# Optimization experiments

Measured on AMD Instinct MI355X. Metric: run time of the kernel, lower is better.

Reference implementation:

```python
import jax, jax.numpy as jnp
import numpy as np

H = 64
NA, NB, NM, NC = 65536, 131072, 16384, 2048
EDGES = {  # name: (E, n_src, n_dst)
    'aa': (786432, NA, NA), 'ab': (262144, NA, NB), 'am': (262144, NA, NM),
    'bb': (786432, NB, NB), 'bm': (524288, NB, NM), 'mm': (131072, NM, NM),
    'ac': (65536,  NA, NC), 'bc': (131072, NB, NC), 'mc': (16384,  NM, NC),
}
REL_ORDER = ['aa', 'ab', 'am', 'bb', 'bm', 'mm', 'ac', 'bc', 'mc']
SRC = {'aa': 'atom', 'ab': 'atom', 'am': 'atom', 'bb': 'bond', 'bm': 'bond',
       'mm': 'motif', 'ac': 'atom', 'bc': 'bond', 'mc': 'motif'}
DST = {'aa': 'atom', 'ab': 'bond', 'am': 'motif', 'bb': 'bond', 'bm': 'motif',
       'mm': 'motif', 'ac': 'cell', 'bc': 'cell', 'mc': 'cell'}
SIZES = {'atom': NA, 'bond': NB, 'motif': NM, 'cell': NC}


def _edge(k, e, n_src, n_dst):
    k1, k2 = jax.random.split(k)
    return jnp.stack([jax.random.randint(k1, (e,), 0, n_src, dtype=jnp.int32),
                      jax.random.randint(k2, (e,), 0, n_dst, dtype=jnp.int32)])


def setup_inputs() -> dict:
    key = jax.random.key(0)
    ks = iter(jax.random.split(key, 32))
    s = 0.05
    inp = {
        'x_atom': jax.random.normal(next(ks), (NA, 92), jnp.float32),
        'x_bond': jax.random.normal(next(ks), (NB, 7), jnp.float32),
        'x_motif': jax.random.normal(next(ks), (NM, 35), jnp.float32),
        'x_cell': jax.random.normal(next(ks), (NC, H), jnp.float32),
        # input projections
        'Wa': jax.random.normal(next(ks), (92, H), jnp.float32) * s,
        'ba': jnp.zeros((H,), jnp.float32),
        'Wb': jax.random.normal(next(ks), (7, H), jnp.float32) * s,
        'bb_': jnp.zeros((H,), jnp.float32),
        'Wm': jax.random.normal(next(ks), (35, H), jnp.float32) * s,
        'bm_': jnp.zeros((H,), jnp.float32),
        # 9 CGConv relations, each lin_f/lin_s: [2H -> H]
        'Wf': jax.random.normal(next(ks), (9, 2 * H, H), jnp.float32) * s,
        'bf': jnp.zeros((9, H), jnp.float32),
        'Ws': jax.random.normal(next(ks), (9, 2 * H, H), jnp.float32) * s,
        'bs': jnp.zeros((9, H), jnp.float32),
        # head
        'Wp': jax.random.normal(next(ks), (H, H), jnp.float32) * s,
        'bp': jnp.zeros((H,), jnp.float32),
        'Wo': jax.random.normal(next(ks), (H, 1), jnp.float32) * s,
        'bo': jnp.zeros((1,), jnp.float32),
    }
    for name in REL_ORDER:
        e, ns, nd = EDGES[name]
        inp['e_' + name] = _edge(next(ks), e, ns, nd)
    return inp


def reference(x_atom, x_bond, x_motif, x_cell,
              Wa, ba, Wb, bb_, Wm, bm_, Wf, bf, Ws, bs, Wp, bp, Wo, bo,
              e_aa, e_ab, e_am, e_bb, e_bm, e_mm, e_ac, e_bc, e_mc):
    edges = {'aa': e_aa, 'ab': e_ab, 'am': e_am, 'bb': e_bb, 'bm': e_bm,
             'mm': e_mm, 'ac': e_ac, 'bc': e_bc, 'mc': e_mc}
    x = {'atom': x_atom @ Wa + ba,
         'bond': x_bond @ Wb + bb_,
         'motif': x_motif @ Wm + bm_,
         'cell': x_cell}
    # one HeteroConv layer (n_layers=1), aggr='sum' across relations per dst type
    new = {k: jnp.zeros_like(v) for k, v in x.items()}
    for r, name in enumerate(REL_ORDER):
        e = edges[name]
        src, dst = SRC[name], DST[name]
        xi = x[dst][e[1]]              # [E, H] target features (x_i)
        xj = x[src][e[0]]              # [E, H] source features (x_j)
        z = jnp.concatenate([xi, xj], axis=-1)  # [E, 2H]
        msg = jax.nn.sigmoid(z @ Wf[r] + bf[r]) * jax.nn.softplus(z @ Ws[r] + bs[r])
        agg = jax.ops.segment_sum(msg, e[1], num_segments=SIZES[dst])
        new[dst] = new[dst] + agg + x[dst]  # CGConv residual, summed over relations
    x = {k: jax.nn.relu(v) for k, v in new.items()}
    h = jax.nn.softplus(x['cell'] @ Wp + bp)
    return h @ Wo + bo  # [NC, 1]
```

## Files before the change

kernel.cpp:

```cpp
#include <hip/hip_runtime.h>
#include <hip/hip_fp16.h>

#define H 64
#define NA 65536
#define NB 131072
#define NM 16384
#define NC 2048
#define E_AC 65536
#define E_BC 131072
#define E_MC 16384
#define NE_TOT (E_AC + E_BC + E_MC)

#define CAPA 160
#define CAPB 224
#define CAPM 96
#define SLOTB (NC * CAPA)
#define SLOTM (SLOTB + NC * CAPB)
#define SLOT_TOT (SLOTM + NC * CAPM)

typedef __attribute__((ext_vector_type(8))) short bf16x8;
typedef __attribute__((ext_vector_type(4))) float f32x4;

__device__ __forceinline__ float sigmoidf_(float x) { return 1.0f / (1.0f + __expf(-x)); }
__device__ __forceinline__ float softplusf_(float x) {
    return fmaxf(x, 0.0f) + __logf(1.0f + __expf(-fabsf(x)));
}
__device__ __forceinline__ short bf16_of(float f) {
    union { float f; unsigned u; } v; v.f = f;
    unsigned r = (v.u + 0x7fff + ((v.u >> 16) & 1)) >> 16;
    return (short)r;
}

__device__ __forceinline__ size_t pack_pos(int k, int col, int S) {
    int part = col >> 6, c = col & 63;
    int t = (c & 3) + part * 4;
    int lo = c >> 2;
    int sm = k >> 5, q = (k >> 3) & 3, e = k & 7;
    return (size_t)(((t * S + sm) * 64) + q * 16 + lo) * 8 + e;
}

__global__ __launch_bounds__(256) void prep0_kernel(
    const float* __restrict__ Wa, const float* __restrict__ ba,
    const float* __restrict__ Wb, const float* __restrict__ bb_,
    const float* __restrict__ Wm, const float* __restrict__ bm,
    const float* __restrict__ Wf, const float* __restrict__ bf,
    const float* __restrict__ Ws, const float* __restrict__ bs,
    short* __restrict__ wpA, short* __restrict__ wpM, short* __restrict__ wpB,
    short* __restrict__ wpC,
    float* __restrict__ biasA, float* __restrict__ biasM, float* __restrict__ biasB,
    float* __restrict__ biasC, int* __restrict__ cnt)
{
    int b = blockIdx.x, tid = threadIdx.x;
    for (int i = b * 256 + tid; i < 3 * NC; i += gridDim.x * 256) cnt[i] = 0;

    if (b < 48) {
        int idx = b * 256 + tid;
        int k = idx >> 7, col = idx & 127, c = col & 63;
        const float* WB = ((col < 64) ? Wf : Ws) + (size_t)6 * 2 * H * H + (size_t)H * H;
        float v = 0.0f;
        if (k < 92) {
            const float* a = Wa + (size_t)k * H;
            for (int j = 0; j < H; ++j) v = fmaf(a[j], WB[j * H + c], v);
        }
        wpA[pack_pos(k, col, 3)] = bf16_of(v);
    } else if (b < 80) {
        int idx = (b - 48) * 256 + tid;
        int k = idx >> 7, col = idx & 127, c = col & 63;
        const float* WB = ((col < 64) ? Wf : Ws) + (size_t)8 * 2 * H * H + (size_t)H * H;
        float v = 0.0f;
        if (k < 35) {
            const float* a = Wm + (size_t)k * H;
            for (int j = 0; j < H; ++j) v = fmaf(a[j], WB[j * H + c], v);
        }
        wpM[pack_pos(k, col, 2)] = bf16_of(v);
    } else if (b < 176) {
        int cu = b - 80;
        int rel = cu >> 5;
        int idx = (cu & 31) * 256 + tid;
        int k = idx >> 7, col = idx & 127, c = col & 63;
        float v = ((col < 64) ? Wf : Ws)[(size_t)(6 + rel) * 2 * H * H + (size_t)k * H + c];
        wpC[(size_t)rel * 8192 + pack_pos(k, col, 2)] = bf16_of(v);
    } else if (b < 192) {
        int idx = (b - 176) * 256 + tid;
        int k = idx >> 7, col = idx & 127, c = col & 63;
        const float* WB = ((col < 64) ? Wf : Ws) + (size_t)7 * 2 * H * H + (size_t)H * H;
        float v = 0.0f;
        if (k < 7) {
            const float* a = Wb + (size_t)k * H;
            for (int j = 0; j < H; ++j) v = fmaf(a[j], WB[j * H + c], v);
        }
        wpB[pack_pos(k, col, 1)] = bf16_of(v);
    } else if (b == 192) {
        if (tid < 128) {
            int col = tid, c = col & 63;
            const float* WB = ((col < 64) ? Wf : Ws) + (size_t)6 * 2 * H * H + (size_t)H * H;
            float v = 0.0f;
            for (int j = 0; j < H; ++j) v = fmaf(ba[j], WB[j * H + c], v);
            biasA[col] = v;
        }
    } else if (b == 193) {
        if (tid < 128) {
            int col = tid, c = col & 63;
            const float* WB = ((col < 64) ? Wf : Ws) + (size_t)8 * 2 * H * H + (size_t)H * H;
            float v = 0.0f;
            for (int j = 0; j < H; ++j) v = fmaf(bm[j], WB[j * H + c], v);
            biasM[col] = v;
        }
    } else if (b == 194) {
        if (tid < 128) {
            int col = tid, c = col & 63;
            const float* WB = ((col < 64) ? Wf : Ws) + (size_t)7 * 2 * H * H + (size_t)H * H;
            float v = 0.0f;
            for (int j = 0; j < H; ++j) v = fmaf(bb_[j], WB[j * H + c], v);
            biasB[col] = v;
        }
    } else {
        for (int i = tid; i < 384; i += 256) {
            int rel = i >> 7, col = i & 127, c = col & 63;
            biasC[rel * 128 + col] = ((col < 64) ? bf : bs)[(6 + rel) * H + c];
        }
    }
}

template<int K, int S, bool VEC>
__device__ __forceinline__ void gmfma_body(
    int blk, const float* __restrict__ x, const short* __restrict__ wp,
    const float* __restrict__ bias, __half2* __restrict__ g)
{
    int l = threadIdx.x & 63;
    int wv = threadIdx.x >> 6;
    int r0 = (blk * 4 + wv) * 16;
    int lrow = l & 15, q = l >> 4;

    float bF[4], bS[4];
    #pragma unroll
    for (int t = 0; t < 4; ++t) {
        bF[t] = bias[lrow * 4 + t];
        bS[t] = bias[64 + lrow * 4 + t];
    }

    f32x4 acc[8];
    #pragma unroll
    for (int t = 0; t < 8; ++t) acc[t] = (f32x4){0.f, 0.f, 0.f, 0.f};

    const float* xr = x + (size_t)(r0 + lrow) * K;
    #pragma unroll
    for (int s = 0; s < S; ++s) {
        int kb = s * 32 + q * 8;
        bf16x8 afrag;
        if (VEC && kb + 8 <= K) {
            float4 v0 = *(const float4*)(xr + kb);
            float4 v1 = *(const float4*)(xr + kb + 4);
            afrag[0] = bf16_of(v0.x); afrag[1] = bf16_of(v0.y);
            afrag[2] = bf16_of(v0.z); afrag[3] = bf16_of(v0.w);
            afrag[4] = bf16_of(v1.x); afrag[5] = bf16_of(v1.y);
            afrag[6] = bf16_of(v1.z); afrag[7] = bf16_of(v1.w);
        } else {
            #pragma unroll
            for (int e = 0; e < 8; ++e) {
                float xv = 0.0f;
                if (kb + e < K) xv = xr[kb + e];
                afrag[e] = bf16_of(xv);
            }
        }
        #pragma unroll
        for (int t = 0; t < 8; ++t) {
            bf16x8 bt = *(const bf16x8*)(wp + (size_t)((t * S + s) * 64 + l) * 8);
            acc[t] = __builtin_amdgcn_mfma_f32_16x16x32_bf16(afrag, bt, acc[t], 0, 0, 0);
        }
    }

    #pragma unroll
    for (int r = 0; r < 4; ++r) {
        __half2 h[4];
        #pragma unroll
        for (int t = 0; t < 4; ++t)
            h[t] = __floats2half2_rn(acc[t][r] + bF[t], acc[t + 4][r] + bS[t]);
        *(float4*)(g + (size_t)(r0 + q * 4 + r) * H + lrow * 4) = *(float4*)h;
    }
}

__global__ __launch_bounds__(256) void work_kernel(
    const float* __restrict__ xa, const float* __restrict__ xb, const float* __restrict__ xm,
    const float* __restrict__ xc,
    const short* __restrict__ wpA, const float* __restrict__ biasA,
    const short* __restrict__ wpM, const float* __restrict__ biasM,
    const short* __restrict__ wpB, const float* __restrict__ biasB,
    const short* __restrict__ wpC, const float* __restrict__ biasC,
    const int* __restrict__ ea, const int* __restrict__ eb, const int* __restrict__ em,
    int* __restrict__ cnt, int* __restrict__ slots,
    __half2* __restrict__ gAll, __half2* __restrict__ Ccomb)
{
    int b = blockIdx.x, tid = threadIdx.x;
    if (b < 104) {
        int t0 = b * 256 + tid;
        #pragma unroll
        for (int u2 = 0; u2 < 8; ++u2) {
            int i = t0 + u2 * 26624;
            int r, d, s;
            if (i < E_AC)             { r = 0; s = ea[i];                      d = ea[E_AC + i]; }
            else if (i < E_AC + E_BC) { int k = i - E_AC; r = 1; s = NA + eb[k]; d = eb[E_BC + k]; }
            else                      { int k = i - E_AC - E_BC; r = 2; s = NA + NB + em[k]; d = em[E_MC + k]; }
            int pos = atomicAdd(&cnt[r * NC + d], 1);
            int base, cap;
            if (r == 0)      { base = d * CAPA;         cap = CAPA; }
            else if (r == 1) { base = SLOTB + d * CAPB; cap = CAPB; }
            else             { base = SLOTM + d * CAPM; cap = CAPM; }
            if (pos < cap) slots[base + pos] = s;
        }
    } else if (b < 200) {
        int cu = b - 104;
        int rel = cu >> 5, blk = cu & 31;
        gmfma_body<64, 2, true>(blk, xc, wpC + (size_t)rel * 8192, biasC + rel * 128,
                                Ccomb + (size_t)rel * NC * H);
    } else if (b < 1224) {
        gmfma_body<92, 3, true>(b - 200, xa, wpA, biasA, gAll);
    } else if (b < 3272) {
        gmfma_body<7, 1, false>(b - 1224, xb, wpB, biasB, gAll + (size_t)NA * H);
    } else {
        gmfma_body<35, 2, false>(b - 3272, xm, wpM, biasM, gAll + (size_t)(NA + NB) * H);
    }
}

__global__ __launch_bounds__(512) void cellacc_kernel(
    const __half2* __restrict__ gAll,
    const int* __restrict__ slots, const int* __restrict__ cnt,
    const __half2* __restrict__ Ccomb, const float* __restrict__ xc,
    const float* __restrict__ Wp, const float* __restrict__ bp,
    const float* __restrict__ Wo, const float* __restrict__ bo,
    float* __restrict__ out)
{
    __shared__ int   sL[CAPA + CAPB + CAPM];
    __shared__ float red[8][H];
    __shared__ float vL[H];
    int d = blockIdx.x;
    int tid = threadIdx.x, lane = tid & 63, wv = tid >> 6;

    int nA = min(cnt[d], CAPA);
    int nB = min(cnt[NC + d], CAPB);
    int nM = min(cnt[2 * NC + d], CAPM);
    for (int i = tid; i < nA; i += 512) sL[i] = slots[d * CAPA + i];
    for (int i = tid; i < nB; i += 512) sL[nA + i] = slots[SLOTB + d * CAPB + i];
    for (int i = tid; i < nM; i += 512) sL[nA + nB + i] = slots[SLOTM + d * CAPM + i];
    float2 ccA = __half22float2(Ccomb[(size_t)d * H + lane]);
    float2 ccB = __half22float2(Ccomb[(size_t)(NC + d) * H + lane]);
    float2 ccM = __half22float2(Ccomb[(size_t)(2 * NC + d) * H + lane]);
    __syncthreads();

    int ntot = nA + nB + nM, nAB = nA + nB;
    float acc = 0.0f;
    int cs = (ntot + 7) >> 3;
    int p0 = wv * cs, p1 = min(p0 + cs, ntot);
    for (int p = p0; p < p1; p += 4) {
        float ccx[4], ccy[4], msk[4]; float2 av[4];
        #pragma unroll
        for (int v = 0; v < 4; ++v) {
            int pc = p + v;
            msk[v] = (pc < p1) ? 1.0f : 0.0f;
            pc = min(pc, ntot - 1);
            int row = sL[pc];
            ccx[v] = (pc < nA) ? ccA.x : (pc < nAB) ? ccB.x : ccM.x;
            ccy[v] = (pc < nA) ? ccA.y : (pc < nAB) ? ccB.y : ccM.y;
            av[v] = __half22float2(gAll[(size_t)row * H + lane]);
        }
        #pragma unroll
        for (int v = 0; v < 4; ++v)
            acc += msk[v] * (sigmoidf_(ccx[v] + av[v].x) * softplusf_(ccy[v] + av[v].y));
    }

    red[wv][lane] = acc;
    __syncthreads();
    if (wv == 0) {
        float a = 3.0f * xc[(size_t)d * H + lane];
        #pragma unroll
        for (int w = 0; w < 8; ++w) a += red[w][lane];
        vL[lane] = fmaxf(a, 0.0f);
        __builtin_amdgcn_s_waitcnt(0);
        float aj = bp[lane];
        #pragma unroll
        for (int k = 0; k < H; ++k) aj = fmaf(vL[k], Wp[k * H + lane], aj);
        float contrib = softplusf_(aj) * Wo[lane];
        #pragma unroll
        for (int o = 32; o > 0; o >>= 1) contrib += __shfl_down(contrib, o, 64);
        if (lane == 0) out[d] = contrib + bo[0];
    }
}

extern "C" void kernel_launch(void* const* d_in, const int* in_sizes, int n_in,
                              void* d_out, int out_size, void* d_ws, size_t ws_size,
                              hipStream_t stream)
{
    const float* xa = (const float*)d_in[0];
    const float* xb = (const float*)d_in[1];
    const float* xm = (const float*)d_in[2];
    const float* xc = (const float*)d_in[3];
    const float* Wa = (const float*)d_in[4];
    const float* ba = (const float*)d_in[5];
    const float* Wb = (const float*)d_in[6];
    const float* bb_ = (const float*)d_in[7];
    const float* Wm = (const float*)d_in[8];
    const float* bm = (const float*)d_in[9];
    const float* Wf = (const float*)d_in[10];
    const float* bf = (const float*)d_in[11];
    const float* Ws = (const float*)d_in[12];
    const float* bs = (const float*)d_in[13];
    const float* Wp = (const float*)d_in[14];
    const float* bp = (const float*)d_in[15];
    const float* Wo = (const float*)d_in[16];
    const float* bo = (const float*)d_in[17];
    const int* ea = (const int*)d_in[24];
    const int* eb = (const int*)d_in[25];
    const int* em = (const int*)d_in[26];

    char* base = (char*)d_ws;
    size_t o = 0;
    auto alloc = [&](size_t bytes) { char* r = base + o; o = (o + bytes + 255) & ~(size_t)255; return r; };
    int*     cnt   = (int*)    alloc(3 * NC * sizeof(int));
    int*     slots = (int*)    alloc(SLOT_TOT * sizeof(int));
    short*   wpA   = (short*)  alloc(8 * 3 * 64 * 8 * sizeof(short));
    short*   wpM   = (short*)  alloc(8 * 2 * 64 * 8 * sizeof(short));
    short*   wpB   = (short*)  alloc(8 * 1 * 64 * 8 * sizeof(short));
    short*   wpC   = (short*)  alloc(3 * 8192 * sizeof(short));
    float*   biasA = (float*)  alloc(128 * sizeof(float));
    float*   biasM = (float*)  alloc(128 * sizeof(float));
    float*   biasB = (float*)  alloc(128 * sizeof(float));
    float*   biasC = (float*)  alloc(384 * sizeof(float));
    __half2* Ccomb = (__half2*)alloc((size_t)3 * NC * H * sizeof(__half2));
    __half2* gAll  = (__half2*)alloc((size_t)(NA + NB + NM) * H * sizeof(__half2));
    float*   out   = (float*)d_out;

    prep0_kernel<<<196, 256, 0, stream>>>(Wa, ba, Wb, bb_, Wm, bm, Wf, bf, Ws, bs,
                                          wpA, wpM, wpB, wpC,
                                          biasA, biasM, biasB, biasC, cnt);
    work_kernel<<<3528, 256, 0, stream>>>(xa, xb, xm, xc,
                                          wpA, biasA, wpM, biasM, wpB, biasB, wpC, biasC,
                                          ea, eb, em, cnt, slots, gAll, Ccomb);
    cellacc_kernel<<<NC, 512, 0, stream>>>(gAll, slots, cnt, Ccomb,
                                           xc, Wp, bp, Wo, bo, out);
}
```

Before: 71.05 us.

## Compute bond-to-cell messages on the fly from packed bond inputs

Bond source projections are no longer precomputed for all 131072 bonds with MFMA into a 64-wide half2 buffer. Instead, prep packs each 7-feature bond row into 8 bf16 values, and the cell accumulation kernel computes the 7-term dot product per bc edge using an 8x64 combined weight/bias table. This removes a large GEMM and its writes and reads. In exchange the cell kernel does extra FMAs per bond edge, and the cell loop is split into three per-relation segments.

```diff
diff --git a/kernel.cpp b/kernel.cpp
--- a/kernel.cpp
+++ b/kernel.cpp
@@ -30,6 +30,10 @@
     unsigned r = (v.u + 0x7fff + ((v.u >> 16) & 1)) >> 16;
     return (short)r;
 }
+__device__ __forceinline__ float bf16_to_f(short h) {
+    union { unsigned u; float f; } v; v.u = ((unsigned)(unsigned short)h) << 16;
+    return v.f;
+}
 
 __device__ __forceinline__ size_t pack_pos(int k, int col, int S) {
     int part = col >> 6, c = col & 63;
@@ -40,21 +44,31 @@
 }
 
 __global__ __launch_bounds__(256) void prep0_kernel(
+    const float* __restrict__ xb,
     const float* __restrict__ Wa, const float* __restrict__ ba,
     const float* __restrict__ Wb, const float* __restrict__ bb_,
     const float* __restrict__ Wm, const float* __restrict__ bm,
     const float* __restrict__ Wf, const float* __restrict__ bf,
     const float* __restrict__ Ws, const float* __restrict__ bs,
-    short* __restrict__ wpA, short* __restrict__ wpM, short* __restrict__ wpB,
-    short* __restrict__ wpC,
-    float* __restrict__ biasA, float* __restrict__ biasM, float* __restrict__ biasB,
-    float* __restrict__ biasC, int* __restrict__ cnt)
+    short* __restrict__ xb8,
+    short* __restrict__ wpA, short* __restrict__ wpM, short* __restrict__ wpC,
+    float* __restrict__ biasA, float* __restrict__ biasM, float* __restrict__ biasC,
+    __half2* __restrict__ WcB, int* __restrict__ cnt)
 {
     int b = blockIdx.x, tid = threadIdx.x;
     for (int i = b * 256 + tid; i < 3 * NC; i += gridDim.x * 256) cnt[i] = 0;
 
-    if (b < 48) {
-        int idx = b * 256 + tid;
+    if (b < 128) {
+        for (int r = b * 1024 + tid; r < b * 1024 + 1024; r += 256) {
+            const float* p = xb + (size_t)r * 7;
+            bf16x8 h;
+            #pragma unroll
+            for (int k = 0; k < 7; ++k) h[k] = bf16_of(p[k]);
+            h[7] = 0;
+            *(bf16x8*)(xb8 + (size_t)r * 8) = h;
+        }
+    } else if (b < 176) {
+        int idx = (b - 128) * 256 + tid;
         int k = idx >> 7, col = idx & 127, c = col & 63;
         const float* WB = ((col < 64) ? Wf : Ws) + (size_t)6 * 2 * H * H + (size_t)H * H;
         float v = 0.0f;
@@ -63,8 +77,8 @@
             for (int j = 0; j < H; ++j) v = fmaf(a[j], WB[j * H + c], v);
         }
         wpA[pack_pos(k, col, 3)] = bf16_of(v);
-    } else if (b < 80) {
-        int idx = (b - 48) * 256 + tid;
+    } else if (b < 208) {
+        int idx = (b - 176) * 256 + tid;
         int k = idx >> 7, col = idx & 127, c = col & 63;
         const float* WB = ((col < 64) ? Wf : Ws) + (size_t)8 * 2 * H * H + (size_t)H * H;
         float v = 0.0f;
@@ -73,24 +87,14 @@
             for (int j = 0; j < H; ++j) v = fmaf(a[j], WB[j * H + c], v);
         }
         wpM[pack_pos(k, col, 2)] = bf16_of(v);
-    } else if (b < 176) {
-        int cu = b - 80;
+    } else if (b < 304) {
+        int cu = b - 208;
         int rel = cu >> 5;
         int idx = (cu & 31) * 256 + tid;
         int k = idx >> 7, col = idx & 127, c = col & 63;
         float v = ((col < 64) ? Wf : Ws)[(size_t)(6 + rel) * 2 * H * H + (size_t)k * H + c];
         wpC[(size_t)rel * 8192 + pack_pos(k, col, 2)] = bf16_of(v);
-    } else if (b < 192) {
-        int idx = (b - 176) * 256 + tid;
-        int k = idx >> 7, col = idx & 127, c = col & 63;
-        const float* WB = ((col < 64) ? Wf : Ws) + (size_t)7 * 2 * H * H + (size_t)H * H;
-        float v = 0.0f;
-        if (k < 7) {
-            const float* a = Wb + (size_t)k * H;
-            for (int j = 0; j < H; ++j) v = fmaf(a[j], WB[j * H + c], v);
-        }
-        wpB[pack_pos(k, col, 1)] = bf16_of(v);
-    } else if (b == 192) {
+    } else if (b == 304) {
         if (tid < 128) {
             int col = tid, c = col & 63;
             const float* WB = ((col < 64) ? Wf : Ws) + (size_t)6 * 2 * H * H + (size_t)H * H;
@@ -98,7 +102,7 @@
             for (int j = 0; j < H; ++j) v = fmaf(ba[j], WB[j * H + c], v);
             biasA[col] = v;
         }
-    } else if (b == 193) {
+    } else if (b == 305) {
         if (tid < 128) {
             int col = tid, c = col & 63;
             const float* WB = ((col < 64) ? Wf : Ws) + (size_t)8 * 2 * H * H + (size_t)H * H;
@@ -106,18 +110,25 @@
             for (int j = 0; j < H; ++j) v = fmaf(bm[j], WB[j * H + c], v);
             biasM[col] = v;
         }
-    } else if (b == 194) {
-        if (tid < 128) {
-            int col = tid, c = col & 63;
-            const float* WB = ((col < 64) ? Wf : Ws) + (size_t)7 * 2 * H * H + (size_t)H * H;
-            float v = 0.0f;
-            for (int j = 0; j < H; ++j) v = fmaf(bb_[j], WB[j * H + c], v);
-            biasB[col] = v;
-        }
-    } else {
+    } else if (b == 306) {
         for (int i = tid; i < 384; i += 256) {
             int rel = i >> 7, col = i & 127, c = col & 63;
             biasC[rel * 128 + col] = ((col < 64) ? bf : bs)[(6 + rel) * H + c];
+        }
+    } else {
+        int idx = (b - 307) * 256 + tid;
+        if (idx < 8 * 64) {
+            int k = idx >> 6, col = idx & 63;
+            const float* WfB = Wf + (size_t)7 * 2 * H * H + (size_t)H * H;
+            const float* WsB = Ws + (size_t)7 * 2 * H * H + (size_t)H * H;
+            const float* row = (k < 7) ? (Wb + (size_t)k * H) : bb_;
+            float f = 0.0f, s = 0.0f;
+            for (int j = 0; j < H; ++j) {
+                float rv = row[j];
+                f = fmaf(rv, WfB[j * H + col], f);
+                s = fmaf(rv, WsB[j * H + col], s);
+            }
+            WcB[k * 64 + col] = __floats2half2_rn(f, s);
         }
     }
 }
@@ -181,11 +192,9 @@
 }
 
 __global__ __launch_bounds__(256) void work_kernel(
-    const float* __restrict__ xa, const float* __restrict__ xb, const float* __restrict__ xm,
-    const float* __restrict__ xc,
+    const float* __restrict__ xa, const float* __restrict__ xm, const float* __restrict__ xc,
     const short* __restrict__ wpA, const float* __restrict__ biasA,
     const short* __restrict__ wpM, const float* __restrict__ biasM,
-    const short* __restrict__ wpB, const float* __restrict__ biasB,
     const short* __restrict__ wpC, const float* __restrict__ biasC,
     const int* __restrict__ ea, const int* __restrict__ eb, const int* __restrict__ em,
     int* __restrict__ cnt, int* __restrict__ slots,
@@ -198,9 +207,9 @@
         for (int u2 = 0; u2 < 8; ++u2) {
             int i = t0 + u2 * 26624;
             int r, d, s;
-            if (i < E_AC)             { r = 0; s = ea[i];                      d = ea[E_AC + i]; }
-            else if (i < E_AC + E_BC) { int k = i - E_AC; r = 1; s = NA + eb[k]; d = eb[E_BC + k]; }
-            else                      { int k = i - E_AC - E_BC; r = 2; s = NA + NB + em[k]; d = em[E_MC + k]; }
+            if (i < E_AC)             { r = 0; s = ea[i];                 d = ea[E_AC + i]; }
+            else if (i < E_AC + E_BC) { int k = i - E_AC; r = 1; s = eb[k]; d = eb[E_BC + k]; }
+            else                      { int k = i - E_AC - E_BC; r = 2; s = NA + em[k]; d = em[E_MC + k]; }
             int pos = atomicAdd(&cnt[r * NC + d], 1);
             int base, cap;
             if (r == 0)      { base = d * CAPA;         cap = CAPA; }
@@ -215,15 +224,14 @@
                                 Ccomb + (size_t)rel * NC * H);
     } else if (b < 1224) {
         gmfma_body<92, 3, true>(b - 200, xa, wpA, biasA, gAll);
-    } else if (b < 3272) {
-        gmfma_body<7, 1, false>(b - 1224, xb, wpB, biasB, gAll + (size_t)NA * H);
     } else {
-        gmfma_body<35, 2, false>(b - 3272, xm, wpM, biasM, gAll + (size_t)(NA + NB) * H);
+        gmfma_body<35, 2, false>(b - 1224, xm, wpM, biasM, gAll + (size_t)NA * H);
     }
 }
 
 __global__ __launch_bounds__(512) void cellacc_kernel(
-    const __half2* __restrict__ gAll,
+    const __half2* __restrict__ gAll, const short* __restrict__ xb8,
+    const __half2* __restrict__ WcB,
     const int* __restrict__ slots, const int* __restrict__ cnt,
     const __half2* __restrict__ Ccomb, const float* __restrict__ xc,
     const float* __restrict__ Wp, const float* __restrict__ bp,
@@ -245,27 +253,74 @@
     float2 ccA = __half22float2(Ccomb[(size_t)d * H + lane]);
     float2 ccB = __half22float2(Ccomb[(size_t)(NC + d) * H + lane]);
     float2 ccM = __half22float2(Ccomb[(size_t)(2 * NC + d) * H + lane]);
+    float wcf[8], wcs[8];
+    #pragma unroll
+    for (int k = 0; k < 8; ++k) {
+        float2 w = __half22float2(WcB[k * 64 + lane]);
+        wcf[k] = w.x; wcs[k] = w.y;
+    }
     __syncthreads();
 
     int ntot = nA + nB + nM, nAB = nA + nB;
     float acc = 0.0f;
     int cs = (ntot + 7) >> 3;
     int p0 = wv * cs, p1 = min(p0 + cs, ntot);
-    for (int p = p0; p < p1; p += 4) {
-        float ccx[4], ccy[4], msk[4]; float2 av[4];
-        #pragma unroll
-        for (int v = 0; v < 4; ++v) {
-            int pc = p + v;
-            msk[v] = (pc < p1) ? 1.0f : 0.0f;
-            pc = min(pc, ntot - 1);
-            int row = sL[pc];
-            ccx[v] = (pc < nA) ? ccA.x : (pc < nAB) ? ccB.x : ccM.x;
-            ccy[v] = (pc < nA) ? ccA.y : (pc < nAB) ? ccB.y : ccM.y;
-            av[v] = __half22float2(gAll[(size_t)row * H + lane]);
-        }
-        #pragma unroll
-        for (int v = 0; v < 4; ++v)
-            acc += msk[v] * (sigmoidf_(ccx[v] + av[v].x) * softplusf_(ccy[v] + av[v].y));
+
+    {
+        int a1 = min(p1, nA);
+        for (int p = p0; p < a1; p += 4) {
+            float msk[4]; float2 av[4];
+            #pragma unroll
+            for (int v = 0; v < 4; ++v) {
+                int pc = p + v;
+                msk[v] = (pc < a1) ? 1.0f : 0.0f;
+                int row = sL[min(pc, a1 - 1)];
+                av[v] = __half22float2(gAll[(size_t)row * H + lane]);
+            }
+            #pragma unroll
+            for (int v = 0; v < 4; ++v)
+                acc += msk[v] * (sigmoidf_(ccA.x + av[v].x) * softplusf_(ccA.y + av[v].y));
+        }
+    }
+    {
+        int b0 = max(p0, nA), b1 = min(p1, nAB);
+        for (int p = b0; p < b1; p += 4) {
+            float msk[4]; bf16x8 xr[4];
+            #pragma unroll
+            for (int v = 0; v < 4; ++v) {
+                int pc = p + v;
+                msk[v] = (pc < b1) ? 1.0f : 0.0f;
+                int row = sL[min(pc, b1 - 1)];
+                xr[v] = *(const bf16x8*)(xb8 + (size_t)row * 8);
+            }
+            #pragma unroll
+            for (int v = 0; v < 4; ++v) {
+                float gf = wcf[7], gs = wcs[7];
+                #pragma unroll
+                for (int k = 0; k < 7; ++k) {
+                    float xv = bf16_to_f(xr[v][k]);
+                    gf = fmaf(xv, wcf[k], gf);
+                    gs = fmaf(xv, wcs[k], gs);
+                }
+                acc += msk[v] * (sigmoidf_(ccB.x + gf) * softplusf_(ccB.y + gs));
+            }
+        }
+    }
+    {
+        int m0 = max(p0, nAB);
+        for (int p = m0; p < p1; p += 4) {
+            float msk[4]; float2 av[4];
+            #pragma unroll
+            for (int v = 0; v < 4; ++v) {
+                int pc = p + v;
+                msk[v] = (pc < p1) ? 1.0f : 0.0f;
+                int row = sL[min(pc, p1 - 1)];
+                av[v] = __half22float2(gAll[(size_t)row * H + lane]);
+            }
+            #pragma unroll
+            for (int v = 0; v < 4; ++v)
+                acc += msk[v] * (sigmoidf_(ccM.x + av[v].x) * softplusf_(ccM.y + av[v].y));
+        }
     }
 
     red[wv][lane] = acc;
@@ -317,24 +372,23 @@
     auto alloc = [&](size_t bytes) { char* r = base + o; o = (o + bytes + 255) & ~(size_t)255; return r; };
     int*     cnt   = (int*)    alloc(3 * NC * sizeof(int));
     int*     slots = (int*)    alloc(SLOT_TOT * sizeof(int));
+    short*   xb8   = (short*)  alloc((size_t)NB * 8 * sizeof(short));
     short*   wpA   = (short*)  alloc(8 * 3 * 64 * 8 * sizeof(short));
     short*   wpM   = (short*)  alloc(8 * 2 * 64 * 8 * sizeof(short));
-    short*   wpB   = (short*)  alloc(8 * 1 * 64 * 8 * sizeof(short));
     short*   wpC   = (short*)  alloc(3 * 8192 * sizeof(short));
     float*   biasA = (float*)  alloc(128 * sizeof(float));
     float*   biasM = (float*)  alloc(128 * sizeof(float));
-    float*   biasB = (float*)  alloc(128 * sizeof(float));
     float*   biasC = (float*)  alloc(384 * sizeof(float));
+    __half2* WcB   = (__half2*)alloc(8 * 64 * sizeof(__half2));
     __half2* Ccomb = (__half2*)alloc((size_t)3 * NC * H * sizeof(__half2));
-    __half2* gAll  = (__half2*)alloc((size_t)(NA + NB + NM) * H * sizeof(__half2));
+    __half2* gAll  = (__half2*)alloc((size_t)(NA + NM) * H * sizeof(__half2));
     float*   out   = (float*)d_out;
 
-    prep0_kernel<<<196, 256, 0, stream>>>(Wa, ba, Wb, bb_, Wm, bm, Wf, bf, Ws, bs,
-                                          wpA, wpM, wpB, wpC,
-                                          biasA, biasM, biasB, biasC, cnt);
-    work_kernel<<<3528, 256, 0, stream>>>(xa, xb, xm, xc,
-                                          wpA, biasA, wpM, biasM, wpB, biasB, wpC, biasC,
+    prep0_kernel<<<309, 256, 0, stream>>>(xb, Wa, ba, Wb, bb_, Wm, bm, Wf, bf, Ws, bs,
+                                          xb8, wpA, wpM, wpC, biasA, biasM, biasC, WcB, cnt);
+    work_kernel<<<1480, 256, 0, stream>>>(xa, xm, xc,
+                                          wpA, biasA, wpM, biasM, wpC, biasC,
                                           ea, eb, em, cnt, slots, gAll, Ccomb);
-    cellacc_kernel<<<NC, 512, 0, stream>>>(gAll, slots, cnt, Ccomb,
+    cellacc_kernel<<<NC, 512, 0, stream>>>(gAll, xb8, WcB, slots, cnt, Ccomb,
                                            xc, Wp, bp, Wo, bo, out);
 }
```

New measurement: 71.59 us. Within noise of the previous version (+0.8%).
